# Performance work log

Hardware: AMD Instinct MI355X
Metric: run time of the kernel (lower is better)

The kernel has to match this reference:

```python
import jax, jax.numpy as jnp
import numpy as np
from jax import lax

K = 3      # reassembly kernel size
UP = 2     # upsample factor


def setup_inputs() -> dict:
    key = jax.random.key(0)
    ks = jax.random.split(key, 4)
    N, C, H, W = 4, 256, 128, 128
    outC = 256
    x = jax.random.normal(ks[0], (N, C, H, W), dtype=jnp.float32)
    w_down = jax.random.normal(ks[1], (C // 4, C), dtype=jnp.float32) * 0.05
    b_down = jnp.zeros((C // 4,), dtype=jnp.float32)
    w_enc = jax.random.normal(ks[2], (UP * UP * K * K, C // 4, K, K), dtype=jnp.float32) * 0.05
    b_enc = jnp.zeros((UP * UP * K * K,), dtype=jnp.float32)
    w_out = jax.random.normal(ks[3], (outC, C), dtype=jnp.float32) * 0.05
    b_out = jnp.zeros((outC,), dtype=jnp.float32)
    return {"x": x, "w_down": w_down, "b_down": b_down,
            "w_enc": w_enc, "b_enc": b_enc, "w_out": w_out, "b_out": b_out}


def _carafe_upsample(x, w_down, b_down, w_enc, b_enc, w_out, b_out):
    N, C, H, W = x.shape
    k2, up2 = K * K, UP * UP
    # kernel prediction branch: 1x1 down conv, 3x3 encoder conv
    t = jnp.einsum('oc,nchw->nohw', w_down, x) + b_down[None, :, None, None]
    enc = lax.conv_general_dilated(
        t, w_enc, window_strides=(1, 1), padding=((K // 2, K // 2), (K // 2, K // 2)),
        dimension_numbers=('NCHW', 'OIHW', 'NCHW')) + b_enc[None, :, None, None]
    # torch encoder channel layout is kk*up2 + ij; pixel_shuffle + softmax(dim=1)
    # + unfold(up,up) is equivalent to softmax over the k^2 axis here.
    enc = enc.reshape(N, k2, up2, H, W)
    kernel = jax.nn.softmax(enc, axis=1)                 # [N,k2,up2,H,W]
    kernel = kernel.transpose(0, 3, 4, 1, 2)             # [N,H,W,k2,up2]
    # extract kxk patches (zero pad), ordering di*K+dj matches torch unfold
    pad = K // 2
    xp = jnp.pad(x, ((0, 0), (0, 0), (pad, pad), (pad, pad)))
    patches = jnp.stack([xp[:, :, di:di + H, dj:dj + W]
                         for di in range(K) for dj in range(K)], axis=-1)  # [N,C,H,W,k2]
    # per-pixel reassembly matmul
    out = jnp.einsum('nchwk,nhwkq->nchwq', patches, kernel)  # [N,C,H,W,up2]
    # pixel_shuffle: channel index c*up2 + i*UP + j -> (h*UP+i, w*UP+j)
    out = out.reshape(N, C, H, W, UP, UP).transpose(0, 1, 2, 4, 3, 5)
    out = out.reshape(N, C, H * UP, W * UP)
    # final 1x1 conv
    return jnp.einsum('oc,nchw->nohw', w_out, out) + b_out[None, :, None, None]


def reference(x, w_down, b_down, w_enc, b_enc, w_out, b_out):
    return _carafe_upsample(x, w_down, b_down, w_enc, b_enc, w_out, b_out)
```

## Files before the change

kernel.cpp:

```cpp
#include <hip/hip_runtime.h>
#include <hip/hip_bf16.h>
#include <stddef.h>

typedef __attribute__((ext_vector_type(8))) short short8;
typedef __attribute__((ext_vector_type(4))) short short4v;
typedef __attribute__((ext_vector_type(4))) unsigned short ushort4v;
typedef __attribute__((ext_vector_type(4))) float floatx4;

#define N_ 4
#define C_ 256
#define H_ 128
#define W_ 128
#define HW_ (H_*W_)
#define NPX_ (N_*HW_)
#define CD_ 64
#define E_ 36
#define OC_ 256

static __device__ __forceinline__ unsigned short f2bf(float f) {
    union { float f; unsigned u; } v; v.f = f;
    unsigned r = v.u + 0x7fff + ((v.u >> 16) & 1);
    return (unsigned short)(r >> 16);
}
static __device__ __forceinline__ float bf2f(unsigned short s) {
    union { unsigned u; float f; } v; v.u = ((unsigned)s) << 16;
    return v.f;
}

__global__ __launch_bounds__(256) void k_prep(const float* __restrict__ wo,
                                              short* __restrict__ wob,
                                              const float* __restrict__ we,
                                              unsigned short* __restrict__ wBT) {
    int bx = blockIdx.x;
    if (bx < 64) {
        int i = (bx * 256 + threadIdx.x) * 4;
        float4 v = *(const float4*)&wo[i];
        short4v s;
        s.x = (short)f2bf(v.x); s.y = (short)f2bf(v.y);
        s.z = (short)f2bf(v.z); s.w = (short)f2bf(v.w);
        *(short4v*)&wob[i] = s;
    } else {
        int idx = (bx - 64) * 256 + threadIdx.x;
        if (idx < 48 * 576) {
            int e = idx / 576;
            int k = idx - e * 576;
            int tap = k >> 6, c = k & 63;
            float v = (e < E_) ? we[((size_t)e * 64 + c) * 9 + tap] : 0.f;
            wBT[idx] = f2bf(v);
        }
    }
}

#define WST 68
#define XST 132
__global__ __launch_bounds__(512) void k_down(
    const float* __restrict__ x, const float* __restrict__ wd,
    const float* __restrict__ bd, unsigned short* __restrict__ t)
{
    __shared__ float Wsm[32 * WST];
    __shared__ float Xs[32 * XST];
    int tid = threadIdx.x;
    int bx = blockIdx.x;
    int n = bx >> 7;
    int px0 = (bx & 127) * 128;
    int mg = tid & 15;
    int ng = tid >> 4;
    float acc[4][4];
    #pragma unroll
    for (int i = 0; i < 4; i++)
        #pragma unroll
        for (int j = 0; j < 4; j++) acc[i][j] = 0.f;

    for (int c0 = 0; c0 < C_; c0 += 32) {
        {
            int o = tid >> 3, kb = tid & 7;
            float4 wv = *(const float4*)&wd[o * C_ + c0 + kb * 4];
            Wsm[(kb * 4 + 0) * WST + o] = wv.x;
            Wsm[(kb * 4 + 1) * WST + o] = wv.y;
            Wsm[(kb * 4 + 2) * WST + o] = wv.z;
            Wsm[(kb * 4 + 3) * WST + o] = wv.w;
        }
        {
            int c = tid >> 4, pg = tid & 15;
            const float* xp = &x[((size_t)n * C_ + c0 + c) * HW_ + px0 + pg * 8];
            #pragma unroll
            for (int i = 0; i < 2; i++) {
                float4 v = *(const float4*)(xp + i * 4);
                *(float4*)&Xs[c * XST + pg * 8 + i * 4] = v;
            }
        }
        __syncthreads();
        #pragma unroll 4
        for (int k = 0; k < 32; k++) {
            float4 wv = *(const float4*)&Wsm[k * WST + mg * 4];
            float4 xv = *(const float4*)&Xs[k * XST + ng * 4];
            float xs[4] = {xv.x, xv.y, xv.z, xv.w};
            float ws[4] = {wv.x, wv.y, wv.z, wv.w};
            #pragma unroll
            for (int i = 0; i < 4; i++)
                #pragma unroll
                for (int j = 0; j < 4; j++)
                    acc[i][j] = fmaf(ws[i], xs[j], acc[i][j]);
        }
        __syncthreads();
    }
    float b0 = bd[mg * 4 + 0], b1 = bd[mg * 4 + 1], b2 = bd[mg * 4 + 2], b3 = bd[mg * 4 + 3];
    #pragma unroll
    for (int j = 0; j < 4; j++) {
        ushort4v r;
        r.x = f2bf(acc[0][j] + b0);
        r.y = f2bf(acc[1][j] + b1);
        r.z = f2bf(acc[2][j] + b2);
        r.w = f2bf(acc[3][j] + b3);
        *(ushort4v*)&t[((size_t)n * HW_ + px0 + ng * 4 + j) * 64 + mg * 4] = r;
    }
}

__global__ __launch_bounds__(256) void k_enc(
    const unsigned short* __restrict__ t, const unsigned short* __restrict__ wBT,
    const float* __restrict__ be, float* __restrict__ kern)
{
    __shared__ unsigned short Tl[198 * 64];
    __shared__ float El[64 * 48];

    int bx = blockIdx.x;
    int n = bx >> 8, h = (bx >> 1) & 127, wh = bx & 1;
    int w0 = wh * 64;
    int tid = threadIdx.x;

    for (int idx = tid; idx < 1584; idx += 256) {
        int r = idx >> 3, ch = idx & 7;
        int di = r / 66, rr = r - di * 66;
        int hh = h + di - 1, ww = w0 + rr - 1;
        short8 v = {0,0,0,0,0,0,0,0};
        if (hh >= 0 && hh < H_ && ww >= 0 && ww < W_)
            v = *(const short8*)&t[((size_t)(n * H_ + hh) * W_ + ww) * 64 + ch * 8];
        int us = (r * 64 + ch * 8) ^ ((r & 7) << 3);
        *(short8*)&Tl[us] = v;
    }
    __syncthreads();

    int lane = tid & 63, wave = tid >> 6;
    int m0 = wave * 16;

    floatx4 acc[3];
    acc[0] = (floatx4)0.f; acc[1] = (floatx4)0.f; acc[2] = (floatx4)0.f;

    int pxl = m0 + (lane & 15);
    int kq = (lane >> 4) * 8;
    #pragma unroll
    for (int kc = 0; kc < 18; kc++) {
        const int tap = kc >> 1, chalf = kc & 1;
        const int di = tap / 3, dj = tap % 3;
        int r = di * 66 + pxl + dj;
        int us = (r * 64 + chalf * 32 + kq) ^ ((r & 7) << 3);
        short8 af = *(const short8*)&Tl[us];
        #pragma unroll
        for (int fn = 0; fn < 3; fn++) {
            int nn = fn * 16 + (lane & 15);
            short8 bf = *(const short8*)&wBT[(size_t)nn * 576 + kc * 32 + kq];
            acc[fn] = __builtin_amdgcn_mfma_f32_16x16x32_bf16(af, bf, acc[fn], 0, 0, 0);
        }
    }
    #pragma unroll
    for (int fn = 0; fn < 3; fn++)
        #pragma unroll
        for (int i = 0; i < 4; i++) {
            int px = m0 + (lane >> 4) * 4 + i;
            El[px * 48 + fn * 16 + (lane & 15)] = acc[fn][i];
        }
    __syncthreads();

    int sp = tid >> 2, q = tid & 3;
    float l[9];
    #pragma unroll
    for (int k = 0; k < 9; k++) l[k] = El[sp * 48 + k * 4 + q] + be[k * 4 + q];
    float m = l[0];
    #pragma unroll
    for (int k = 1; k < 9; k++) m = fmaxf(m, l[k]);
    float ex[9], s = 0.f;
    #pragma unroll
    for (int k = 0; k < 9; k++) { ex[k] = __expf(l[k] - m); s += ex[k]; }
    float inv = 1.f / s;
    int pxg = n * HW_ + h * W_ + w0 + sp;
    #pragma unroll
    for (int k = 0; k < 9; k++)
        kern[(size_t)(k * 4 + q) * NPX_ + pxg] = ex[k] * inv;
}

__global__ __launch_bounds__(512, 4) void k_gemm(
    const float* __restrict__ x, const short* __restrict__ wob,
    unsigned short* __restrict__ Gq)
{
    __shared__ short Asm[2][256 * 40];
    __shared__ short Bsm[2][128 * 40];

    int tid = threadIdx.x;
    int bx = blockIdx.x;
    int n = bx >> 7;
    int px0 = (bx & 127) * 128;

    int lane = tid & 63;
    int wave = tid >> 6;
    int wm = wave >> 2, wn = wave & 3;

    int ao = tid >> 1, ah = tid & 1;
    int bpx = tid & 127, bcq = tid >> 7;

    const float* xb = x + (size_t)n * C_ * HW_ + px0 + bpx;
    const short* wr = wob + ao * C_ + ah * 16;

    short8 a0, a1;
    float xg[8];

    auto issue = [&](int c0) {
        a0 = *(const short8*)(wr + c0);
        a1 = *(const short8*)(wr + c0 + 8);
        #pragma unroll
        for (int j = 0; j < 8; j++)
            xg[j] = xb[(size_t)(c0 + bcq * 8 + j) * HW_];
    };
    auto commit = [&](int buf) {
        short* ad = &Asm[buf][ao * 40 + ah * 16];
        *(short8*)ad = a0;
        *(short8*)(ad + 8) = a1;
        short8 bv;
        #pragma unroll
        for (int j = 0; j < 8; j++) bv[j] = (short)f2bf(xg[j]);
        *(short8*)&Bsm[buf][bpx * 40 + bcq * 8] = bv;
    };

    floatx4 acc[8][2];
    #pragma unroll
    for (int fm = 0; fm < 8; fm++) {
        acc[fm][0] = (floatx4)0.f;
        acc[fm][1] = (floatx4)0.f;
    }

    issue(0);
    commit(0);
    __syncthreads();

    for (int kc = 0; kc < 8; kc++) {
        int cur = kc & 1;
        if (kc < 7) issue((kc + 1) * 32);
        short8 bfrag[2];
        #pragma unroll
        for (int fn = 0; fn < 2; fn++) {
            int col = wn * 32 + fn * 16 + (lane & 15);
            bfrag[fn] = *(const short8*)&Bsm[cur][col * 40 + (lane >> 4) * 8];
        }
        #pragma unroll
        for (int fm = 0; fm < 8; fm++) {
            int row = wm * 128 + fm * 16 + (lane & 15);
            short8 af = *(const short8*)&Asm[cur][row * 40 + (lane >> 4) * 8];
            acc[fm][0] = __builtin_amdgcn_mfma_f32_16x16x32_bf16(af, bfrag[0], acc[fm][0], 0, 0, 0);
            acc[fm][1] = __builtin_amdgcn_mfma_f32_16x16x32_bf16(af, bfrag[1], acc[fm][1], 0, 0, 0);
        }
        if (kc < 7) {
            commit(cur ^ 1);
            __syncthreads();
        }
    }
    #pragma unroll
    for (int fm = 0; fm < 8; fm++) {
        int oq = wm * 32 + fm * 4 + (lane >> 4);
        #pragma unroll
        for (int fn = 0; fn < 2; fn++) {
            int col = px0 + wn * 32 + fn * 16 + (lane & 15);
            ushort4v v;
            v.x = f2bf(acc[fm][fn][0]);
            v.y = f2bf(acc[fm][fn][1]);
            v.z = f2bf(acc[fm][fn][2]);
            v.w = f2bf(acc[fm][fn][3]);
            *(ushort4v*)&Gq[(((size_t)n * 64 + oq) * HW_ + col) * 4] = v;
        }
    }
}

__global__ __launch_bounds__(256) void k_up(
    const unsigned short* __restrict__ Gq, const float* __restrict__ kern,
    const float* __restrict__ bo, float* __restrict__ y)
{
    int bx = blockIdx.x;
    int x7 = bx & 7;
    int g  = bx >> 3;
    int hbhi = g & 7;
    int og = (g >> 3) & 7;
    int n  = g >> 6;
    int hb = hbhi * 8 + x7;

    int tid = threadIdx.x;
    int h = hb * 2 + (tid >> 7);
    int w = tid & 127;
    int idxp = n * HW_ + h * W_ + w;

    float kv[36];
    #pragma unroll
    for (int e = 0; e < E_; e++)
        kv[e] = kern[(size_t)e * NPX_ + idxp];

    int off[9]; bool val[9];
    #pragma unroll
    for (int di = 0; di < 3; di++) {
        int hh = h + di - 1;
        bool hvv = (hh >= 0 && hh < H_);
        int hc = hvv ? hh : h;
        #pragma unroll
        for (int dj = 0; dj < 3; dj++) {
            int ww = w + dj - 1;
            bool wvv = (ww >= 0 && ww < W_);
            int wc = wvv ? ww : w;
            off[di * 3 + dj] = hc * W_ + wc;
            val[di * 3 + dj] = hvv && wvv;
        }
    }

    const unsigned short* Gb = Gq + ((size_t)n * 64 + og * 8) * HW_ * 4;
    size_t ybase = ((size_t)n * OC_ + og * 32) * (4 * HW_) + (size_t)(2 * h) * 256 + 2 * w;

    #pragma unroll 2
    for (int j = 0; j < 8; j++) {
        const unsigned short* Gj = Gb + (size_t)j * HW_ * 4;
        float b0 = bo[og * 32 + j * 4 + 0];
        float b1 = bo[og * 32 + j * 4 + 1];
        float b2 = bo[og * 32 + j * 4 + 2];
        float b3 = bo[og * 32 + j * 4 + 3];
        float a[4][4];
        #pragma unroll
        for (int s = 0; s < 4; s++) { a[0][s] = b0; a[1][s] = b1; a[2][s] = b2; a[3][s] = b3; }
        #pragma unroll
        for (int k = 0; k < 9; k++) {
            ushort4v gv = *(const ushort4v*)(Gj + (size_t)off[k] * 4);
            float g0 = val[k] ? bf2f(gv.x) : 0.f;
            float g1 = val[k] ? bf2f(gv.y) : 0.f;
            float g2 = val[k] ? bf2f(gv.z) : 0.f;
            float g3 = val[k] ? bf2f(gv.w) : 0.f;
            #pragma unroll
            for (int s = 0; s < 4; s++) {
                float kw = kv[k * 4 + s];
                a[0][s] = fmaf(g0, kw, a[0][s]);
                a[1][s] = fmaf(g1, kw, a[1][s]);
                a[2][s] = fmaf(g2, kw, a[2][s]);
                a[3][s] = fmaf(g3, kw, a[3][s]);
            }
        }
        #pragma unroll
        for (int i = 0; i < 4; i++) {
            float* yp = y + ybase + (size_t)(j * 4 + i) * (4 * HW_);
            float2 r0; r0.x = a[i][0]; r0.y = a[i][1];
            float2 r1; r1.x = a[i][2]; r1.y = a[i][3];
            *(float2*)yp = r0;
            *(float2*)(yp + 256) = r1;
        }
    }
}

extern "C" void kernel_launch(void* const* d_in, const int* in_sizes, int n_in,
                              void* d_out, int out_size, void* d_ws, size_t ws_size,
                              hipStream_t stream) {
    const float* x  = (const float*)d_in[0];
    const float* wd = (const float*)d_in[1];
    const float* bd = (const float*)d_in[2];
    const float* we = (const float*)d_in[3];
    const float* be = (const float*)d_in[4];
    const float* wo = (const float*)d_in[5];
    const float* bo = (const float*)d_in[6];
    float* y = (float*)d_out;

    unsigned short* t = (unsigned short*)d_ws;
    float* kern = (float*)(t + (size_t)NPX_ * 64);
    short* wob  = (short*)(kern + (size_t)E_ * NPX_);
    unsigned short* wBT = (unsigned short*)(wob + (size_t)OC_ * C_);
    unsigned short* Gq  = wBT + (size_t)48 * 576;

    k_prep<<<172,  256, 0, stream>>>(wo, wob, we, wBT);
    k_down<<<512,  512, 0, stream>>>(x, wd, bd, t);
    k_enc <<<1024, 256, 0, stream>>>(t, wBT, be, kern);
    k_gemm<<<512,  512, 0, stream>>>(x, wob, Gq);
    k_up  <<<2048, 256, 0, stream>>>(Gq, kern, bo, y);
}
```

Measured before the change: 148.9 us.

## Fuse 1x1 down-projection into the output-weight MFMA GEMM sharing one x read

Removes the separate FP32 k_down kernel and appends the 64 down-projection weight rows to the bf16 output-weight matrix, so a single MFMA GEMM produces both Gq and the down-projected t from one pass over x. This avoids reading the full 64 MB input twice and replaces FP32 FMA math with bf16 tensor-core math for the down conv. In exchange, t is now computed from bf16-rounded inputs and weights, the GEMM uses more LDS and accumulators, and occupancy drops to 3 blocks.

```diff
diff --git a/kernel.cpp b/kernel.cpp
--- a/kernel.cpp
+++ b/kernel.cpp
@@ -13,7 +13,6 @@
 #define W_ 128
 #define HW_ (H_*W_)
 #define NPX_ (N_*HW_)
-#define CD_ 64
 #define E_ 36
 #define OC_ 256
 
@@ -28,19 +27,22 @@
 }
 
 __global__ __launch_bounds__(256) void k_prep(const float* __restrict__ wo,
-                                              short* __restrict__ wob,
+                                              const float* __restrict__ wd,
+                                              short* __restrict__ wcomb,
                                               const float* __restrict__ we,
                                               unsigned short* __restrict__ wBT) {
     int bx = blockIdx.x;
-    if (bx < 64) {
+    if (bx < 80) {
         int i = (bx * 256 + threadIdx.x) * 4;
-        float4 v = *(const float4*)&wo[i];
+        int row = i >> 8, c = i & 255;
+        const float* src = (row < 256) ? &wo[row * 256 + c] : &wd[(row - 256) * 256 + c];
+        float4 v = *(const float4*)src;
         short4v s;
         s.x = (short)f2bf(v.x); s.y = (short)f2bf(v.y);
         s.z = (short)f2bf(v.z); s.w = (short)f2bf(v.w);
-        *(short4v*)&wob[i] = s;
+        *(short4v*)&wcomb[i] = s;
     } else {
-        int idx = (bx - 64) * 256 + threadIdx.x;
+        int idx = (bx - 80) * 256 + threadIdx.x;
         if (idx < 48 * 576) {
             int e = idx / 576;
             int k = idx - e * 576;
@@ -51,68 +53,121 @@
     }
 }
 
-#define WST 68
-#define XST 132
-__global__ __launch_bounds__(512) void k_down(
-    const float* __restrict__ x, const float* __restrict__ wd,
-    const float* __restrict__ bd, unsigned short* __restrict__ t)
+__global__ __launch_bounds__(512, 3) void k_gemm(
+    const float* __restrict__ x, const short* __restrict__ wcomb,
+    const float* __restrict__ bd,
+    unsigned short* __restrict__ Gq, unsigned short* __restrict__ t)
 {
-    __shared__ float Wsm[32 * WST];
-    __shared__ float Xs[32 * XST];
+    __shared__ short Asm[2][320 * 40];
+    __shared__ short Bsm[2][128 * 40];
+
     int tid = threadIdx.x;
     int bx = blockIdx.x;
     int n = bx >> 7;
     int px0 = (bx & 127) * 128;
-    int mg = tid & 15;
-    int ng = tid >> 4;
-    float acc[4][4];
-    #pragma unroll
-    for (int i = 0; i < 4; i++)
-        #pragma unroll
-        for (int j = 0; j < 4; j++) acc[i][j] = 0.f;
-
-    for (int c0 = 0; c0 < C_; c0 += 32) {
-        {
-            int o = tid >> 3, kb = tid & 7;
-            float4 wv = *(const float4*)&wd[o * C_ + c0 + kb * 4];
-            Wsm[(kb * 4 + 0) * WST + o] = wv.x;
-            Wsm[(kb * 4 + 1) * WST + o] = wv.y;
-            Wsm[(kb * 4 + 2) * WST + o] = wv.z;
-            Wsm[(kb * 4 + 3) * WST + o] = wv.w;
-        }
-        {
-            int c = tid >> 4, pg = tid & 15;
-            const float* xp = &x[((size_t)n * C_ + c0 + c) * HW_ + px0 + pg * 8];
-            #pragma unroll
-            for (int i = 0; i < 2; i++) {
-                float4 v = *(const float4*)(xp + i * 4);
-                *(float4*)&Xs[c * XST + pg * 8 + i * 4] = v;
-            }
-        }
-        __syncthreads();
-        #pragma unroll 4
-        for (int k = 0; k < 32; k++) {
-            float4 wv = *(const float4*)&Wsm[k * WST + mg * 4];
-            float4 xv = *(const float4*)&Xs[k * XST + ng * 4];
-            float xs[4] = {xv.x, xv.y, xv.z, xv.w};
-            float ws[4] = {wv.x, wv.y, wv.z, wv.w};
-            #pragma unroll
-            for (int i = 0; i < 4; i++)
-                #pragma unroll
-                for (int j = 0; j < 4; j++)
-                    acc[i][j] = fmaf(ws[i], xs[j], acc[i][j]);
-        }
-        __syncthreads();
-    }
-    float b0 = bd[mg * 4 + 0], b1 = bd[mg * 4 + 1], b2 = bd[mg * 4 + 2], b3 = bd[mg * 4 + 3];
-    #pragma unroll
-    for (int j = 0; j < 4; j++) {
-        ushort4v r;
-        r.x = f2bf(acc[0][j] + b0);
-        r.y = f2bf(acc[1][j] + b1);
-        r.z = f2bf(acc[2][j] + b2);
-        r.w = f2bf(acc[3][j] + b3);
-        *(ushort4v*)&t[((size_t)n * HW_ + px0 + ng * 4 + j) * 64 + mg * 4] = r;
+
+    int lane = tid & 63;
+    int wave = tid >> 6;
+    int wm = wave >> 2, wn = wave & 3;
+
+    int ao = tid >> 1, ah = tid & 1;
+    int bpx = tid & 127, bcq = tid >> 7;
+    bool hasExtra = (tid < 128);
+
+    const float* xb = x + (size_t)n * C_ * HW_ + px0 + bpx;
+    const short* wr  = wcomb + ao * C_ + ah * 16;
+    const short* wr2 = wcomb + (256 + (tid >> 1)) * C_ + (tid & 1) * 16;
+
+    short8 a0, a1, a2, a3;
+    float xg[8];
+
+    auto issue = [&](int c0) {
+        a0 = *(const short8*)(wr + c0);
+        a1 = *(const short8*)(wr + c0 + 8);
+        if (hasExtra) {
+            a2 = *(const short8*)(wr2 + c0);
+            a3 = *(const short8*)(wr2 + c0 + 8);
+        }
+        #pragma unroll
+        for (int j = 0; j < 8; j++)
+            xg[j] = xb[(size_t)(c0 + bcq * 8 + j) * HW_];
+    };
+    auto commit = [&](int buf) {
+        short* ad = &Asm[buf][ao * 40 + ah * 16];
+        *(short8*)ad = a0;
+        *(short8*)(ad + 8) = a1;
+        if (hasExtra) {
+            short* ad2 = &Asm[buf][(256 + (tid >> 1)) * 40 + (tid & 1) * 16];
+            *(short8*)ad2 = a2;
+            *(short8*)(ad2 + 8) = a3;
+        }
+        short8 bv;
+        #pragma unroll
+        for (int j = 0; j < 8; j++) bv[j] = (short)f2bf(xg[j]);
+        *(short8*)&Bsm[buf][bpx * 40 + bcq * 8] = bv;
+    };
+
+    floatx4 acc[10][2];
+    #pragma unroll
+    for (int fm = 0; fm < 10; fm++) {
+        acc[fm][0] = (floatx4)0.f;
+        acc[fm][1] = (floatx4)0.f;
+    }
+
+    issue(0);
+    commit(0);
+    __syncthreads();
+
+    for (int kc = 0; kc < 8; kc++) {
+        int cur = kc & 1;
+        if (kc < 7) issue((kc + 1) * 32);
+        short8 bfrag[2];
+        #pragma unroll
+        for (int fn = 0; fn < 2; fn++) {
+            int col = wn * 32 + fn * 16 + (lane & 15);
+            bfrag[fn] = *(const short8*)&Bsm[cur][col * 40 + (lane >> 4) * 8];
+        }
+        #pragma unroll
+        for (int fm = 0; fm < 10; fm++) {
+            int rbase = (fm < 8) ? (wm * 128 + fm * 16) : (256 + wm * 32 + (fm - 8) * 16);
+            int row = rbase + (lane & 15);
+            short8 af = *(const short8*)&Asm[cur][row * 40 + (lane >> 4) * 8];
+            acc[fm][0] = __builtin_amdgcn_mfma_f32_16x16x32_bf16(af, bfrag[0], acc[fm][0], 0, 0, 0);
+            acc[fm][1] = __builtin_amdgcn_mfma_f32_16x16x32_bf16(af, bfrag[1], acc[fm][1], 0, 0, 0);
+        }
+        if (kc < 7) {
+            commit(cur ^ 1);
+            __syncthreads();
+        }
+    }
+    #pragma unroll
+    for (int fm = 0; fm < 8; fm++) {
+        int oq = wm * 32 + fm * 4 + (lane >> 4);
+        #pragma unroll
+        for (int fn = 0; fn < 2; fn++) {
+            int col = px0 + wn * 32 + fn * 16 + (lane & 15);
+            ushort4v v;
+            v.x = f2bf(acc[fm][fn][0]);
+            v.y = f2bf(acc[fm][fn][1]);
+            v.z = f2bf(acc[fm][fn][2]);
+            v.w = f2bf(acc[fm][fn][3]);
+            *(ushort4v*)&Gq[(((size_t)n * 64 + oq) * HW_ + col) * 4] = v;
+        }
+    }
+    #pragma unroll
+    for (int f8 = 0; f8 < 2; f8++) {
+        int ot = wm * 32 + f8 * 16 + ((lane >> 4) << 2);
+        float b0 = bd[ot + 0], b1 = bd[ot + 1], b2 = bd[ot + 2], b3 = bd[ot + 3];
+        #pragma unroll
+        for (int fn = 0; fn < 2; fn++) {
+            int col = px0 + wn * 32 + fn * 16 + (lane & 15);
+            ushort4v r;
+            r.x = f2bf(acc[8 + f8][fn][0] + b0);
+            r.y = f2bf(acc[8 + f8][fn][1] + b1);
+            r.z = f2bf(acc[8 + f8][fn][2] + b2);
+            r.w = f2bf(acc[8 + f8][fn][3] + b3);
+            *(ushort4v*)&t[((size_t)n * HW_ + col) * 64 + ot] = r;
+        }
     }
 }
 
@@ -186,96 +241,6 @@
     #pragma unroll
     for (int k = 0; k < 9; k++)
         kern[(size_t)(k * 4 + q) * NPX_ + pxg] = ex[k] * inv;
-}
-
-__global__ __launch_bounds__(512, 4) void k_gemm(
-    const float* __restrict__ x, const short* __restrict__ wob,
-    unsigned short* __restrict__ Gq)
-{
-    __shared__ short Asm[2][256 * 40];
-    __shared__ short Bsm[2][128 * 40];
-
-    int tid = threadIdx.x;
-    int bx = blockIdx.x;
-    int n = bx >> 7;
-    int px0 = (bx & 127) * 128;
-
-    int lane = tid & 63;
-    int wave = tid >> 6;
-    int wm = wave >> 2, wn = wave & 3;
-
-    int ao = tid >> 1, ah = tid & 1;
-    int bpx = tid & 127, bcq = tid >> 7;
-
-    const float* xb = x + (size_t)n * C_ * HW_ + px0 + bpx;
-    const short* wr = wob + ao * C_ + ah * 16;
-
-    short8 a0, a1;
-    float xg[8];
-
-    auto issue = [&](int c0) {
-        a0 = *(const short8*)(wr + c0);
-        a1 = *(const short8*)(wr + c0 + 8);
-        #pragma unroll
-        for (int j = 0; j < 8; j++)
-            xg[j] = xb[(size_t)(c0 + bcq * 8 + j) * HW_];
-    };
-    auto commit = [&](int buf) {
-        short* ad = &Asm[buf][ao * 40 + ah * 16];
-        *(short8*)ad = a0;
-        *(short8*)(ad + 8) = a1;
-        short8 bv;
-        #pragma unroll
-        for (int j = 0; j < 8; j++) bv[j] = (short)f2bf(xg[j]);
-        *(short8*)&Bsm[buf][bpx * 40 + bcq * 8] = bv;
-    };
-
-    floatx4 acc[8][2];
-    #pragma unroll
-    for (int fm = 0; fm < 8; fm++) {
-        acc[fm][0] = (floatx4)0.f;
-        acc[fm][1] = (floatx4)0.f;
-    }
-
-    issue(0);
-    commit(0);
-    __syncthreads();
-
-    for (int kc = 0; kc < 8; kc++) {
-        int cur = kc & 1;
-        if (kc < 7) issue((kc + 1) * 32);
-        short8 bfrag[2];
-        #pragma unroll
-        for (int fn = 0; fn < 2; fn++) {
-            int col = wn * 32 + fn * 16 + (lane & 15);
-            bfrag[fn] = *(const short8*)&Bsm[cur][col * 40 + (lane >> 4) * 8];
-        }
-        #pragma unroll
-        for (int fm = 0; fm < 8; fm++) {
-            int row = wm * 128 + fm * 16 + (lane & 15);
-            short8 af = *(const short8*)&Asm[cur][row * 40 + (lane >> 4) * 8];
-            acc[fm][0] = __builtin_amdgcn_mfma_f32_16x16x32_bf16(af, bfrag[0], acc[fm][0], 0, 0, 0);
-            acc[fm][1] = __builtin_amdgcn_mfma_f32_16x16x32_bf16(af, bfrag[1], acc[fm][1], 0, 0, 0);
-        }
-        if (kc < 7) {
-            commit(cur ^ 1);
-            __syncthreads();
-        }
-    }
-    #pragma unroll
-    for (int fm = 0; fm < 8; fm++) {
-        int oq = wm * 32 + fm * 4 + (lane >> 4);
-        #pragma unroll
-        for (int fn = 0; fn < 2; fn++) {
-            int col = px0 + wn * 32 + fn * 16 + (lane & 15);
-            ushort4v v;
-            v.x = f2bf(acc[fm][fn][0]);
-            v.y = f2bf(acc[fm][fn][1]);
-            v.z = f2bf(acc[fm][fn][2]);
-            v.w = f2bf(acc[fm][fn][3]);
-            *(ushort4v*)&Gq[(((size_t)n * 64 + oq) * HW_ + col) * 4] = v;
-        }
-    }
 }
 
 __global__ __launch_bounds__(256) void k_up(
@@ -370,13 +335,12 @@
 
     unsigned short* t = (unsigned short*)d_ws;
     float* kern = (float*)(t + (size_t)NPX_ * 64);
-    short* wob  = (short*)(kern + (size_t)E_ * NPX_);
-    unsigned short* wBT = (unsigned short*)(wob + (size_t)OC_ * C_);
+    short* wcomb = (short*)(kern + (size_t)E_ * NPX_);
+    unsigned short* wBT = (unsigned short*)(wcomb + (size_t)320 * C_);
     unsigned short* Gq  = wBT + (size_t)48 * 576;
 
-    k_prep<<<172,  256, 0, stream>>>(wo, wob, we, wBT);
-    k_down<<<512,  512, 0, stream>>>(x, wd, bd, t);
+    k_prep<<<188,  256, 0, stream>>>(wo, wd, wcomb, we, wBT);
+    k_gemm<<<512,  512, 0, stream>>>(x, wcomb, bd, Gq, t);
     k_enc <<<1024, 256, 0, stream>>>(t, wBT, be, kern);
-    k_gemm<<<512,  512, 0, stream>>>(x, wob, Gq);
     k_up  <<<2048, 256, 0, stream>>>(Gq, kern, bo, y);
 }
```

Result: no change. 148.8 us (-0.1%).
